# Kernel tuning notes

Hardware: AMD Instinct MI355X
Metric: run time of the kernel (lower is better)

## Reference

```python
import jax, jax.numpy as jnp
import numpy as np

EMBED = 768
HEAD = 256

def setup_inputs() -> dict:
    key = jax.random.key(0)
    k1, k2, k3, k4 = jax.random.split(key, 4)
    res_stream = jax.random.normal(k1, (512, 128, EMBED), dtype=jnp.float32)
    # torch Linear(embed, head, bias=False): y = x @ W.T, W: [head, embed].
    # Store as [embed, head] so y = x @ W.
    Wk = jax.random.normal(k2, (EMBED, HEAD), dtype=jnp.float32) * (EMBED ** -0.5)
    Wq = jax.random.normal(k3, (EMBED, HEAD), dtype=jnp.float32) * (EMBED ** -0.5)
    Wv = jax.random.normal(k4, (EMBED, HEAD), dtype=jnp.float32) * (EMBED ** -0.5)
    return {"res_stream": res_stream, "Wk": Wk, "Wq": Wq, "Wv": Wv}

def reference(res_stream, Wk, Wq, Wv):
    B, T, E = res_stream.shape
    q = jnp.einsum('bte,eh->bth', res_stream, Wq)  # [B,T,H]
    k = jnp.einsum('bte,eh->bth', res_stream, Wk)
    v = jnp.einsum('bte,eh->bth', res_stream, Wv)
    # NOTE: original scales by embed**-0.5 (not head_size**-0.5)
    scores = jnp.einsum('bth,bsh->bts', q, k) * (E ** -0.5)  # [B,T,T]
    causal = jnp.tril(jnp.ones((T, T), dtype=bool))
    scores = jnp.where(causal, scores, -jnp.inf)
    attn = jax.nn.softmax(scores, axis=-1)
    # dropout: eval mode (identity) for deterministic reference
    return jnp.einsum('bts,bsh->bth', attn, v)  # [B,T,H]
```

## Files before the change

kernel.cpp:

```cpp
#include <hip/hip_runtime.h>
#include <hip/hip_bf16.h>

typedef float f32x4 __attribute__((ext_vector_type(4)));
typedef short bfx8 __attribute__((ext_vector_type(8)));

typedef const __attribute__((address_space(1))) void* gvp;
typedef __attribute__((address_space(3))) void* lvp;

static __device__ __forceinline__ unsigned short f2bf(float f) {
    return __builtin_bit_cast(unsigned short, __float2bfloat16(f));
}

static __device__ __forceinline__ bfx8 cvt8(f32x4 lo, f32x4 hi) {
    bfx8 r;
    r[0] = (short)f2bf(lo[0]); r[1] = (short)f2bf(lo[1]);
    r[2] = (short)f2bf(lo[2]); r[3] = (short)f2bf(lo[3]);
    r[4] = (short)f2bf(hi[0]); r[5] = (short)f2bf(hi[1]);
    r[6] = (short)f2bf(hi[2]); r[7] = (short)f2bf(hi[3]);
    return r;
}

__global__ void prep_w(const float* __restrict__ Wk, const float* __restrict__ Wq,
                       const float* __restrict__ Wv, unsigned short* __restrict__ WT) {
    const int n = blockIdx.x;
    const int e = threadIdx.x;
    const int which = n >> 8;
    const int h = n & 255;
    const float* W = (which == 0) ? Wq : (which == 1) ? Wk : Wv;
    WT[(size_t)n * 768 + e] = f2bf(W[(size_t)e * 256 + h]);
}

__global__ void cvt_x(const float* __restrict__ X, unsigned short* __restrict__ Xb,
                      long n) {
    long i = ((long)blockIdx.x * 256 + threadIdx.x) * 8;
    const long stride = (long)gridDim.x * 256 * 8;
    for (; i < n; i += stride) {
        f32x4 lo = *(const f32x4*)(X + i);
        f32x4 hi = *(const f32x4*)(X + i + 4);
        *(bfx8*)(Xb + i) = cvt8(lo, hi);
    }
}

__global__ __launch_bounds__(256) void qkv_gemm(const unsigned short* __restrict__ Xb,
                                                const unsigned short* __restrict__ WT,
                                                unsigned short* __restrict__ QKV,
                                                int b0, int nwg) {
    __shared__ unsigned short Ab[128][64];
    __shared__ unsigned short Bb[128][64];

    const int tid = threadIdx.x;
    const int bid = blockIdx.x;
    const int q = nwg >> 3, r = nwg & 7;
    const int xcd = bid & 7, idx = bid >> 3;
    const int l = (xcd < r ? xcd * (q + 1) : r * (q + 1) + (xcd - r) * q) + idx;
    const int bn = l % 6;
    const int bm = l / 6;
    const int m0 = bm * 128;
    const int n0 = bn * 128;
    const int w = tid >> 6, lane = tid & 63;
    const int wr = w >> 1, wc = w & 1;
    const int lrow = lane & 15, lhi = lane >> 4;
    const bool vswap = (bn >= 4);

    f32x4 acc[4][4];
    const f32x4 zero = {0.f, 0.f, 0.f, 0.f};
#pragma unroll
    for (int i = 0; i < 4; ++i)
#pragma unroll
        for (int j = 0; j < 4; ++j) acc[i][j] = zero;

    for (int kt = 0; kt < 12; ++kt) {
        const int k0 = kt * 64;
#pragma unroll
        for (int i = 0; i < 4; ++i) {
            const int f = i * 256 + tid;
            const int row = f >> 3;
            const int cbs = ((f & 7) * 16) ^ ((row & 7) << 4);
            const unsigned short* ga = Xb + (size_t)(m0 + row) * 768 + k0 + (cbs >> 1);
            char* lpa = (char*)&Ab[0][0] + i * 4096 + w * 1024;
            __builtin_amdgcn_global_load_lds((gvp)ga, (lvp)lpa, 16, 0, 0);
            const unsigned short* gb = WT + (size_t)(n0 + row) * 768 + k0 + (cbs >> 1);
            char* lpb = (char*)&Bb[0][0] + i * 4096 + w * 1024;
            __builtin_amdgcn_global_load_lds((gvp)gb, (lvp)lpb, 16, 0, 0);
        }
        __syncthreads();

#pragma unroll
        for (int kk = 0; kk < 2; ++kk) {
            const int kb2 = (kk * 32 + lhi * 8) * 2;
            bfx8 a[4], bb4[4];
#pragma unroll
            for (int mi = 0; mi < 4; ++mi) {
                const int arow = wr * 64 + mi * 16 + lrow;
                a[mi] = *(const bfx8*)((const char*)&Ab[arow][0] +
                                       (kb2 ^ ((arow & 7) << 4)));
            }
#pragma unroll
            for (int ni = 0; ni < 4; ++ni) {
                const int brow = wc * 64 + ni * 16 + lrow;
                bb4[ni] = *(const bfx8*)((const char*)&Bb[brow][0] +
                                         (kb2 ^ ((brow & 7) << 4)));
            }
            if (!vswap) {
#pragma unroll
                for (int mi = 0; mi < 4; ++mi)
#pragma unroll
                    for (int ni = 0; ni < 4; ++ni)
                        acc[mi][ni] = __builtin_amdgcn_mfma_f32_16x16x32_bf16(
                            a[mi], bb4[ni], acc[mi][ni], 0, 0, 0);
            } else {
#pragma unroll
                for (int ni = 0; ni < 4; ++ni)
#pragma unroll
                    for (int mi = 0; mi < 4; ++mi)
                        acc[ni][mi] = __builtin_amdgcn_mfma_f32_16x16x32_bf16(
                            bb4[ni], a[mi], acc[ni][mi], 0, 0, 0);
            }
        }
        __syncthreads();
    }

    const int b = b0 + bm;
    if (!vswap) {
        const int which = bn >> 1;
        const size_t base = ((size_t)(b * 3 + which)) << 15;
        const int hbase = (bn & 1) * 128;
#pragma unroll
        for (int mi = 0; mi < 4; ++mi)
#pragma unroll
            for (int ni = 0; ni < 4; ++ni) {
                const int t = wr * 64 + mi * 16 + lhi * 4;
                const int h = hbase + wc * 64 + ni * 16 + lrow;
#pragma unroll
                for (int j = 0; j < 4; ++j)
                    QKV[base + (size_t)(t + j) * 256 + h] = f2bf(acc[mi][ni][j]);
            }
    } else {
        const size_t base = ((size_t)(b * 3 + 2)) << 15;
#pragma unroll
        for (int ni = 0; ni < 4; ++ni)
#pragma unroll
            for (int mi = 0; mi < 4; ++mi) {
                const int h = (bn - 4) * 128 + wc * 64 + ni * 16 + lhi * 4;
                const int t = wr * 64 + mi * 16 + lrow;
#pragma unroll
                for (int j = 0; j < 4; ++j)
                    QKV[base + (size_t)(h + j) * 128 + t] = f2bf(acc[ni][mi][j]);
            }
    }
}

__global__ __launch_bounds__(512) void attn(const unsigned short* __restrict__ QKV,
                                            float* __restrict__ Out) {
    __shared__ unsigned short Kl[128][264];
    __shared__ unsigned short Vt[256][136];

    const int b = blockIdx.x;
    const int tid = threadIdx.x;
    const int w = tid >> 6, lane = tid & 63;
    const int lrow = lane & 15, lhi = lane >> 4;

    const unsigned short* Qb = QKV + ((size_t)(b * 3 + 0) << 15);
    const unsigned short* Kb = QKV + ((size_t)(b * 3 + 1) << 15);
    const unsigned short* Vb = QKV + ((size_t)(b * 3 + 2) << 15);

    const int t0 = w * 16;
    bfx8 aq[8];
#pragma unroll
    for (int kk = 0; kk < 8; ++kk)
        aq[kk] = *(const bfx8*)(Qb + (size_t)(t0 + lrow) * 256 + kk * 32 + lhi * 8);

#pragma unroll
    for (int i = 0; i < 8; ++i) {
        int f = i * 512 + tid;
        {
            int row = f >> 5, c = (f & 31) * 8;
            *(bfx8*)&Kl[row][c] = *(const bfx8*)(Kb + (size_t)row * 256 + c);
        }
        {
            int row = f >> 4, c = (f & 15) * 8;
            *(bfx8*)&Vt[row][c] = *(const bfx8*)(Vb + (size_t)row * 128 + c);
        }
    }
    __syncthreads();

    f32x4 sacc[8];
    const f32x4 zero = {0.f, 0.f, 0.f, 0.f};
#pragma unroll
    for (int sj = 0; sj < 8; ++sj) sacc[sj] = zero;
#pragma unroll
    for (int kk = 0; kk < 8; ++kk) {
        const int kb = kk * 32 + lhi * 8;
#pragma unroll
        for (int sj = 0; sj < 8; ++sj) {
            bfx8 bk = *(const bfx8*)&Kl[sj * 16 + lrow][kb];
            sacc[sj] = __builtin_amdgcn_mfma_f32_16x16x32_bf16(aq[kk], bk, sacc[sj], 0, 0, 0);
        }
    }

    const float scale = 0.03608439182435161f;
    float inv[4];
#pragma unroll
    for (int j = 0; j < 4; ++j) {
        const int t = t0 + lhi * 4 + j;
        float m = -1e30f;
#pragma unroll
        for (int sj = 0; sj < 8; ++sj) {
            int s = sj * 16 + lrow;
            float vv = sacc[sj][j] * scale;
            vv = (s <= t) ? vv : -1e30f;
            sacc[sj][j] = vv;
            m = fmaxf(m, vv);
        }
#pragma unroll
        for (int d = 1; d < 16; d <<= 1) m = fmaxf(m, __shfl_xor(m, d));
        float sum = 0.f;
#pragma unroll
        for (int sj = 0; sj < 8; ++sj) {
            float e = __expf(sacc[sj][j] - m);
            sacc[sj][j] = e;
            sum += e;
        }
#pragma unroll
        for (int d = 1; d < 16; d <<= 1) sum += __shfl_xor(sum, d);
        inv[j] = 1.0f / sum;
    }

    __syncthreads();

    unsigned short* Pl = &Kl[0][0] + (size_t)w * (16 * 136);
#pragma unroll
    for (int sj = 0; sj < 8; ++sj)
#pragma unroll
        for (int j = 0; j < 4; ++j)
            Pl[(lhi * 4 + j) * 136 + sj * 16 + lrow] = f2bf(sacc[sj][j] * inv[j]);

    bfx8 pa[4];
#pragma unroll
    for (int kk = 0; kk < 4; ++kk)
        pa[kk] = *(const bfx8*)(Pl + lrow * 136 + kk * 32 + lhi * 8);

    f32x4 oacc[16];
#pragma unroll
    for (int ni = 0; ni < 16; ++ni) oacc[ni] = zero;
#pragma unroll
    for (int ni = 0; ni < 16; ++ni) {
#pragma unroll
        for (int kk = 0; kk < 4; ++kk) {
            bfx8 bv = *(const bfx8*)&Vt[ni * 16 + lrow][kk * 32 + lhi * 8];
            oacc[ni] = __builtin_amdgcn_mfma_f32_16x16x32_bf16(pa[kk], bv, oacc[ni], 0, 0, 0);
        }
    }

    float* Ob = Out + (size_t)b * 128 * 256;
#pragma unroll
    for (int ni = 0; ni < 16; ++ni) {
#pragma unroll
        for (int j = 0; j < 4; ++j) {
            const int t = t0 + lhi * 4 + j;
            const int h = ni * 16 + lrow;
            Ob[(size_t)t * 256 + h] = oacc[ni][j];
        }
    }
}

extern "C" void kernel_launch(void* const* d_in, const int* in_sizes, int n_in,
                              void* d_out, int out_size, void* d_ws, size_t ws_size,
                              hipStream_t stream) {
    (void)in_sizes; (void)n_in; (void)out_size;
    const float* X  = (const float*)d_in[0];
    const float* Wk = (const float*)d_in[1];
    const float* Wq = (const float*)d_in[2];
    const float* Wv = (const float*)d_in[3];

    const size_t WT_E  = (size_t)768 * 768;
    const size_t QKV_E = (size_t)512 * 3 * 32768;
    unsigned short* WT  = (unsigned short*)d_ws;
    unsigned short* QKV = WT + WT_E;
    unsigned short* Xb  = QKV + QKV_E;
    float* Out = (float*)d_out;

    const long perBatch = 128 * 768;
    size_t used = (WT_E + QKV_E) * 2;
    size_t availB = (ws_size > used) ? ws_size - used : 0;
    int chunk = (int)((availB / 2) / (size_t)perBatch);
    if (chunk > 512) chunk = 512;
    if (chunk < 1) chunk = 1;

    prep_w<<<768, 768, 0, stream>>>(Wk, Wq, Wv, WT);
    for (int b0 = 0; b0 < 512; b0 += chunk) {
        const int cb = (512 - b0 < chunk) ? (512 - b0) : chunk;
        const long n = (long)cb * perBatch;
        cvt_x<<<2048, 256, 0, stream>>>(X + (size_t)b0 * perBatch, Xb, n);
        const int nwg = cb * 6;
        qkv_gemm<<<nwg, 256, 0, stream>>>(Xb, WT, QKV, b0, nwg);
    }
    attn<<<512, 512, 0, stream>>>(QKV, Out);
}
```

Measured before the change: 218.6 us.

## Double-buffer LDS tiles in QKV GEMM with prefetch two stages ahead

Result: faster. 198.9 us (-9.0%).

```diff
diff --git a/kernel.cpp b/kernel.cpp
--- a/kernel.cpp
+++ b/kernel.cpp
@@ -45,8 +45,7 @@
                                                 const unsigned short* __restrict__ WT,
                                                 unsigned short* __restrict__ QKV,
                                                 int b0, int nwg) {
-    __shared__ unsigned short Ab[128][64];
-    __shared__ unsigned short Bb[128][64];
+    __shared__ __align__(16) char LDS[65536];
 
     const int tid = threadIdx.x;
     const int bid = blockIdx.x;
@@ -69,22 +68,31 @@
 #pragma unroll
         for (int j = 0; j < 4; ++j) acc[i][j] = zero;
 
+#define STAGE(kt, bs)                                                          \
+    {                                                                          \
+        const int k0s = (kt) * 64;                                             \
+        _Pragma("unroll")                                                      \
+        for (int i = 0; i < 4; ++i) {                                          \
+            const int f = i * 256 + tid;                                       \
+            const int row = f >> 3;                                            \
+            const int cbs = ((f & 7) * 16) ^ ((row & 7) << 4);                 \
+            const unsigned short* ga = Xb + (size_t)(m0 + row) * 768 + k0s + (cbs >> 1); \
+            char* lpa = LDS + (bs) * 16384 + i * 4096 + w * 1024;              \
+            __builtin_amdgcn_global_load_lds((gvp)ga, (lvp)lpa, 16, 0, 0);     \
+            const unsigned short* gb = WT + (size_t)(n0 + row) * 768 + k0s + (cbs >> 1); \
+            char* lpb = LDS + 32768 + (bs) * 16384 + i * 4096 + w * 1024;      \
+            __builtin_amdgcn_global_load_lds((gvp)gb, (lvp)lpb, 16, 0, 0);     \
+        }                                                                      \
+    }
+
+    STAGE(0, 0);
+    STAGE(1, 1);
+
+    int cur = 0;
     for (int kt = 0; kt < 12; ++kt) {
-        const int k0 = kt * 64;
-#pragma unroll
-        for (int i = 0; i < 4; ++i) {
-            const int f = i * 256 + tid;
-            const int row = f >> 3;
-            const int cbs = ((f & 7) * 16) ^ ((row & 7) << 4);
-            const unsigned short* ga = Xb + (size_t)(m0 + row) * 768 + k0 + (cbs >> 1);
-            char* lpa = (char*)&Ab[0][0] + i * 4096 + w * 1024;
-            __builtin_amdgcn_global_load_lds((gvp)ga, (lvp)lpa, 16, 0, 0);
-            const unsigned short* gb = WT + (size_t)(n0 + row) * 768 + k0 + (cbs >> 1);
-            char* lpb = (char*)&Bb[0][0] + i * 4096 + w * 1024;
-            __builtin_amdgcn_global_load_lds((gvp)gb, (lvp)lpb, 16, 0, 0);
-        }
-        __syncthreads();
-
+        if (kt < 11) asm volatile("s_waitcnt vmcnt(8)" ::: "memory");
+        else         asm volatile("s_waitcnt vmcnt(0)" ::: "memory");
+        __builtin_amdgcn_s_barrier();
 #pragma unroll
         for (int kk = 0; kk < 2; ++kk) {
             const int kb2 = (kk * 32 + lhi * 8) * 2;
@@ -92,13 +100,13 @@
 #pragma unroll
             for (int mi = 0; mi < 4; ++mi) {
                 const int arow = wr * 64 + mi * 16 + lrow;
-                a[mi] = *(const bfx8*)((const char*)&Ab[arow][0] +
+                a[mi] = *(const bfx8*)(LDS + cur * 16384 + arow * 128 +
                                        (kb2 ^ ((arow & 7) << 4)));
             }
 #pragma unroll
             for (int ni = 0; ni < 4; ++ni) {
                 const int brow = wc * 64 + ni * 16 + lrow;
-                bb4[ni] = *(const bfx8*)((const char*)&Bb[brow][0] +
+                bb4[ni] = *(const bfx8*)(LDS + 32768 + cur * 16384 + brow * 128 +
                                          (kb2 ^ ((brow & 7) << 4)));
             }
             if (!vswap) {
@@ -117,7 +125,9 @@
                             bb4[ni], a[mi], acc[ni][mi], 0, 0, 0);
             }
         }
-        __syncthreads();
+        __builtin_amdgcn_s_barrier();
+        if (kt < 10) STAGE(kt + 2, cur);
+        cur ^= 1;
     }
 
     const int b = b0 + bm;
```
